# Kernel tuning notes

Measured on AMD Instinct MI355X. Metric: run time of the kernel, lower is better.

## Reference

```python
import jax, jax.numpy as jnp
import numpy as np

B, T, N, D = 8, 64, 128, 128  # batch, timesteps, num_nodes, hidden_dim
LN_EPS = 1e-5
L2_EPS = 1e-12


def setup_inputs() -> dict:
    key = jax.random.key(0)
    ks = jax.random.split(key, 8)
    feat = jax.random.normal(ks[0], (B, T, N, D), dtype=jnp.float32)
    w = jax.random.uniform(ks[1], (D,), dtype=jnp.float32)  # learned adj gate (torch.rand init)
    s = 1.0 / np.sqrt(D)
    W1 = jax.random.uniform(ks[2], (D, D), dtype=jnp.float32, minval=-s, maxval=s)
    b1 = jax.random.uniform(ks[3], (D,), dtype=jnp.float32, minval=-s, maxval=s)
    W2 = jax.random.uniform(ks[4], (D, D), dtype=jnp.float32, minval=-s, maxval=s)
    b2 = jax.random.uniform(ks[5], (D,), dtype=jnp.float32, minval=-s, maxval=s)
    gamma = jnp.ones((D,), dtype=jnp.float32)
    beta = jnp.zeros((D,), dtype=jnp.float32)
    return {"feat": feat, "w": w, "W1": W1, "b1": b1, "W2": W2, "b2": b2,
            "gamma": gamma, "beta": beta}


def _windows(x):
    # x: (B, T, N, D) -> (B, T-2, 3*N, D): 3 consecutive timesteps flattened over nodes
    b, t, n, d = x.shape
    return jnp.stack([x[:, i:i + t - 2] for i in range(3)], axis=2).reshape(b, t - 2, 3 * n, d)


def reference(feat, w, W1, b1, W2, b2, gamma, beta):
    # gated + L2-normalized features for learned adjacency
    wf = feat * jax.nn.sigmoid(w)
    wf = wf / jnp.maximum(jnp.linalg.norm(wf, axis=-1, keepdims=True), L2_EPS)

    win = _windows(feat)   # (B, T-2, 3N, D)
    wwin = _windows(wf)    # (B, T-2, 3N, D)

    # learned adjacency: gram matrix per window, (B, T-2, 3N, 3N)
    adj = jnp.einsum('btmd,btnd->btmn', wwin, wwin)

    # symmetric normalization D^{-1/2} A D^{-1/2}; inf/nan (deg<=0) -> 0 as in torch
    deg = adj.sum(axis=-1, keepdims=True)
    dis = jnp.where(deg > 0, jax.lax.rsqrt(jnp.maximum(deg, 1e-38)), 0.0)
    nadj = dis * adj * jnp.swapaxes(dis, -1, -2)

    # message passing, keep last N rows (current timestep)
    agg = jnp.einsum('btmn,btnd->btmd', nadj, win)[:, :, -N:, :]

    # FFN (dropout is identity in eval): Linear -> ReLU -> Linear
    h = jax.nn.relu(agg @ W1 + b1) @ W2 + b2

    # residual with current-timestep features + LayerNorm
    s = feat[:, 2:] + h
    mu = s.mean(axis=-1, keepdims=True)
    var = ((s - mu) ** 2).mean(axis=-1, keepdims=True)
    return (s - mu) * jax.lax.rsqrt(var + LN_EPS) * gamma + beta
```

## Files before the change

### kernel.cpp

```cpp
#include <hip/hip_runtime.h>
#include <math.h>

#define BB    8
#define TDIM  64
#define NN    128
#define DD    128
#define TTOUT 62
#define W3    384
#define LG    136
#define LP    40
#define LW    72

typedef __attribute__((ext_vector_type(8))) short bf16x8;
typedef __attribute__((ext_vector_type(4))) float f32x4;

__device__ __forceinline__ float sigf(float x){ return 1.0f/(1.0f+__expf(-x)); }
__device__ __forceinline__ unsigned short f2bf(float x){
  union{float f; unsigned u;} v; v.f=x;
  unsigned r = v.u + 0x7FFFu + ((v.u>>16)&1u);
  return (unsigned short)(r>>16);
}

__global__ __launch_bounds__(512) void k_pre(const float* __restrict__ feat,
    const float* __restrict__ w, const float* __restrict__ W1, const float* __restrict__ W2,
    float* __restrict__ rscale, float* __restrict__ ssum,
    unsigned short* __restrict__ W1T, unsigned short* __restrict__ W2T){
  __shared__ float sSig[DD];
  __shared__ float sRs[NN];
  __shared__ float sPart[4*DD];
  const int bid = blockIdx.x, tid = threadIdx.x;
  if(bid >= BB*TDIM){
    const float* W = (bid == BB*TDIM) ? W1 : W2;
    unsigned short* WT = (bid == BB*TDIM) ? W1T : W2T;
    for(int e=tid; e<DD*DD; e+=512){
      int k = e>>7, n = e&127;
      WT[n*DD + k] = f2bf(W[(size_t)k*DD + n]);
    }
    return;
  }
  const int bt = bid;
  if(tid < DD) sSig[tid] = sigf(w[tid]);
  __syncthreads();
  const int row = tid >> 2, q = tid & 3;
  const float* fp = feat + ((size_t)bt*NN + row)*DD + q*32;
  float ss = 0.f;
  #pragma unroll
  for(int i=0;i<8;i++){
    float4 v = *(const float4*)(fp + i*4);
    float g0 = v.x*sSig[q*32+i*4+0], g1 = v.y*sSig[q*32+i*4+1];
    float g2 = v.z*sSig[q*32+i*4+2], g3 = v.w*sSig[q*32+i*4+3];
    ss += g0*g0 + g1*g1 + g2*g2 + g3*g3;
  }
  ss += __shfl_xor(ss,1); ss += __shfl_xor(ss,2);
  float rs = 1.0f / fmaxf(sqrtf(ss), 1e-12f);
  if(q==0){ rscale[(size_t)bt*NN + row] = rs; sRs[row] = rs; }
  __syncthreads();
  const int d = tid & 127, rg = tid >> 7;
  const float* fc = feat + ((size_t)bt*NN + rg*32)*DD + d;
  float acc = 0.f;
  #pragma unroll 8
  for(int i=0;i<32;i++) acc += fc[(size_t)i*DD] * sRs[rg*32+i];
  sPart[rg*DD + d] = acc;
  __syncthreads();
  if(tid < DD)
    ssum[(size_t)bt*DD + tid] =
      (sPart[tid] + sPart[DD+tid] + sPart[2*DD+tid] + sPart[3*DD+tid]) * sSig[tid];
}

__global__ __launch_bounds__(512,4) void k_main(
    const float* __restrict__ feat,
    const float* __restrict__ w,
    const float* __restrict__ rscale, const float* __restrict__ ssum,
    const unsigned short* __restrict__ W1T, const float* __restrict__ b1,
    const unsigned short* __restrict__ W2T, const float* __restrict__ b2,
    const float* __restrict__ gamma, const float* __restrict__ beta,
    float* __restrict__ out)
{
  __shared__ __align__(16) unsigned short sm[32000];
  __shared__ float sSig[DD];
  __shared__ float s3c[DD];
  __shared__ float sFac[W3];
  unsigned short* sA  = sm;
  unsigned short* sG  = sm + 17408;
  unsigned short* sFt = sm + 21760;
  unsigned short* sP  = sm + 26880;
  unsigned short* sWt = sm + 17408;

  const int tid = threadIdx.x;
  const int bid = blockIdx.x;
  const int bt2 = (bid & 7)*62 + (bid >> 3);
  const int btIdx = (bt2/TTOUT)*TDIM + (bt2%TTOUT);
  const int rowBase = btIdx * NN;

  const int lane = tid & 63, wid = tid >> 6;
  const int l15 = lane & 15, l4 = lane >> 4;
  const int m0 = wid * 16;

  if(tid < DD){
    float sg = sigf(w[tid]);
    sSig[tid] = sg;
    float s3 = ssum[(size_t)btIdx*DD + tid] + ssum[(size_t)(btIdx+1)*DD + tid]
             + ssum[(size_t)(btIdx+2)*DD + tid];
    s3c[tid] = s3 * sg;
  }
  __syncthreads();

  #pragma unroll
  for(int rg=0; rg<3; ++rg){
    int row = rg*128 + (tid>>2), q = tid&3;
    const float* fpr = feat + (size_t)(rowBase+row)*DD + q*32;
    float a = 0.f;
    #pragma unroll
    for(int i=0;i<8;i++){
      float4 v = *(const float4*)(fpr + i*4);
      const float* sc = s3c + q*32 + i*4;
      a += v.x*sc[0] + v.y*sc[1] + v.z*sc[2] + v.w*sc[3];
    }
    a += __shfl_xor(a,1); a += __shfl_xor(a,2);
    if(q==0){
      float rs = rscale[rowBase+row];
      float deg = a * rs;
      float dis = (deg > 0.f) ? rsqrtf(fmaxf(deg, 1e-38f)) : 0.f;
      sFac[row] = dis * rs;
    }
  }
  __syncthreads();

  #pragma unroll
  for(int e0=0; e0<8; ++e0){
    int e = e0*512 + tid;
    int d = e & 127, r0 = (e>>7)*4;
    float sg = sSig[d];
    #pragma unroll
    for(int i=0;i<4;i++){
      int j = 256 + r0 + i;
      float f = feat[(size_t)(rowBase+j)*DD + d];
      sA[(r0+i)*LG + d] = f2bf(f*sg*sFac[j]);
    }
  }

  f32x4 acc2[8];
  #pragma unroll
  for(int i=0;i<8;i++) acc2[i] = (f32x4){0.f,0.f,0.f,0.f};

  for(int c=0; c<12; ++c){
    const int n0 = c*32;
    __syncthreads();
    #pragma unroll
    for(int e0=0; e0<2; ++e0){
      int e = e0*512 + tid;
      int d = e & 127, r0 = (e>>7)*4;
      float sg = sSig[d];
      unsigned short fb[4];
      #pragma unroll
      for(int i=0;i<4;i++){
        int j = n0 + r0 + i;
        float f = feat[(size_t)(rowBase+j)*DD + d];
        fb[i] = f2bf(f);
        sG[(r0+i)*LG + d] = f2bf(f*sg*sFac[j]);
      }
      unsigned int* fp = (unsigned int*)&sFt[d*LP + r0];
      fp[0] = (unsigned)fb[0] | ((unsigned)fb[1]<<16);
      fp[1] = (unsigned)fb[2] | ((unsigned)fb[3]<<16);
    }
    __syncthreads();

    f32x4 p0 = {0.f,0.f,0.f,0.f}, p1 = {0.f,0.f,0.f,0.f};
    #pragma unroll
    for(int ks=0; ks<4; ++ks){
      bf16x8 aA  = *(const bf16x8*)&sA[(m0+l15)*LG + ks*32 + l4*8];
      bf16x8 bg0 = *(const bf16x8*)&sG[( 0+l15)*LG + ks*32 + l4*8];
      bf16x8 bg1 = *(const bf16x8*)&sG[(16+l15)*LG + ks*32 + l4*8];
      p0 = __builtin_amdgcn_mfma_f32_16x16x32_bf16(aA, bg0, p0, 0,0,0);
      p1 = __builtin_amdgcn_mfma_f32_16x16x32_bf16(aA, bg1, p1, 0,0,0);
    }
    #pragma unroll
    for(int r=0;r<4;r++){
      sP[(m0 + l4*4 + r)*LP +  0 + l15] = f2bf(p0[r]);
      sP[(m0 + l4*4 + r)*LP + 16 + l15] = f2bf(p1[r]);
    }

    bf16x8 aP = *(const bf16x8*)&sP[(m0+l15)*LP + l4*8];
    #pragma unroll
    for(int dt=0; dt<8; ++dt){
      bf16x8 bF = *(const bf16x8*)&sFt[(dt*16+l15)*LP + l4*8];
      acc2[dt] = __builtin_amdgcn_mfma_f32_16x16x32_bf16(aP, bF, acc2[dt], 0,0,0);
    }
  }

  #pragma unroll
  for(int dt=0; dt<8; ++dt)
    #pragma unroll
    for(int r=0;r<4;r++)
      sA[(m0+l4*4+r)*LG + dt*16+l15] = f2bf(acc2[dt][r]);

  f32x4 acch[8];
  #pragma unroll
  for(int dt=0; dt<8; ++dt){
    float bv = b1[dt*16+l15];
    acch[dt] = (f32x4){bv,bv,bv,bv};
  }
  for(int kh=0; kh<2; ++kh){
    __syncthreads();
    #pragma unroll
    for(int it=0; it<2; ++it){
      int e = it*512 + tid, n = e>>3, sg2 = e&7;
      uint4 v = *(const uint4*)(W1T + (size_t)n*DD + kh*64 + sg2*8);
      *(uint4*)&sWt[n*LW + sg2*8] = v;
    }
    __syncthreads();
    #pragma unroll
    for(int ks=0; ks<2; ++ks){
      bf16x8 aA = *(const bf16x8*)&sA[(m0+l15)*LG + kh*64 + ks*32 + l4*8];
      #pragma unroll
      for(int dt=0; dt<8; ++dt){
        bf16x8 bW = *(const bf16x8*)&sWt[(dt*16+l15)*LW + ks*32 + l4*8];
        acch[dt] = __builtin_amdgcn_mfma_f32_16x16x32_bf16(aA, bW, acch[dt], 0,0,0);
      }
    }
  }
  __syncthreads();
  #pragma unroll
  for(int dt=0; dt<8; ++dt)
    #pragma unroll
    for(int r=0;r<4;r++)
      sA[(m0+l4*4+r)*LG + dt*16+l15] = f2bf(fmaxf(acch[dt][r], 0.f));

  f32x4 acco[8];
  #pragma unroll
  for(int dt=0; dt<8; ++dt){
    float bv = b2[dt*16+l15];
    acco[dt] = (f32x4){bv,bv,bv,bv};
  }
  for(int kh=0; kh<2; ++kh){
    __syncthreads();
    #pragma unroll
    for(int it=0; it<2; ++it){
      int e = it*512 + tid, n = e>>3, sg2 = e&7;
      uint4 v = *(const uint4*)(W2T + (size_t)n*DD + kh*64 + sg2*8);
      *(uint4*)&sWt[n*LW + sg2*8] = v;
    }
    __syncthreads();
    #pragma unroll
    for(int ks=0; ks<2; ++ks){
      bf16x8 aA = *(const bf16x8*)&sA[(m0+l15)*LG + kh*64 + ks*32 + l4*8];
      #pragma unroll
      for(int dt=0; dt<8; ++dt){
        bf16x8 bW = *(const bf16x8*)&sWt[(dt*16+l15)*LW + ks*32 + l4*8];
        acco[dt] = __builtin_amdgcn_mfma_f32_16x16x32_bf16(aA, bW, acco[dt], 0,0,0);
      }
    }
  }

  const float* fres = feat + (size_t)(rowBase + 256)*DD;
  #pragma unroll
  for(int r=0;r<4;r++){
    int m = m0 + l4*4 + r;
    float vals[8]; float s1 = 0.f, s2 = 0.f;
    #pragma unroll
    for(int dt=0; dt<8; ++dt){
      int d = dt*16 + l15;
      float v = acco[dt][r] + fres[(size_t)m*DD + d];
      vals[dt] = v; s1 += v; s2 += v*v;
    }
    #pragma unroll
    for(int k=1;k<16;k<<=1){ s1 += __shfl_xor(s1,k); s2 += __shfl_xor(s2,k); }
    float mu   = s1*(1.0f/DD);
    float rstd = rsqrtf(s2*(1.0f/DD) - mu*mu + 1e-5f);
    #pragma unroll
    for(int dt=0; dt<8; ++dt){
      int d = dt*16 + l15;
      out[((size_t)bt2*NN + m)*DD + d] = (vals[dt]-mu)*rstd*gamma[d] + beta[d];
    }
  }
}

extern "C" void kernel_launch(void* const* d_in, const int* in_sizes, int n_in,
                              void* d_out, int out_size, void* d_ws, size_t ws_size,
                              hipStream_t stream){
  const float* feat  = (const float*)d_in[0];
  const float* w     = (const float*)d_in[1];
  const float* W1    = (const float*)d_in[2];
  const float* b1    = (const float*)d_in[3];
  const float* W2    = (const float*)d_in[4];
  const float* b2    = (const float*)d_in[5];
  const float* gamma = (const float*)d_in[6];
  const float* beta  = (const float*)d_in[7];
  float* out = (float*)d_out;

  char* ws = (char*)d_ws;
  float* rscale = (float*)(ws + 0);
  float* ssum   = (float*)(ws + 262144);
  unsigned short* W1T = (unsigned short*)(ws + 524288);
  unsigned short* W2T = (unsigned short*)(ws + 557056);

  k_pre<<<BB*TDIM + 2, 512, 0, stream>>>(feat, w, W1, W2, rscale, ssum, W1T, W2T);
  k_main<<<BB*TTOUT, 512, 0, stream>>>(feat, w, rscale, ssum, W1T, b1, W2T, b2,
                                       gamma, beta, out);
}
```

Measured before the change: 81.36 us.

## Double k_main block to 1024 threads, splitting output columns across wave halves

Each block now runs 16 waves instead of 8. Each pair of waves shares a 16-row strip and splits the output columns (D tiles and the 32-wide P chunk) in half, which halves per-wave accumulator registers and the MFMA work per wave. This aims to raise in-CU parallelism and latency hiding. In exchange it adds one more block-wide barrier per chunk iteration and an LDS round-trip to combine the LayerNorm partial sums across the two halves.

Result: slower. 94.31 us (+15.9%).

```diff
diff --git a/kernel.cpp b/kernel.cpp
--- a/kernel.cpp
+++ b/kernel.cpp
@@ -67,7 +67,7 @@
       (sPart[tid] + sPart[DD+tid] + sPart[2*DD+tid] + sPart[3*DD+tid]) * sSig[tid];
 }
 
-__global__ __launch_bounds__(512,4) void k_main(
+__global__ __launch_bounds__(1024,2) void k_main(
     const float* __restrict__ feat,
     const float* __restrict__ w,
     const float* __restrict__ rscale, const float* __restrict__ ssum,
@@ -80,6 +80,7 @@
   __shared__ float sSig[DD];
   __shared__ float s3c[DD];
   __shared__ float sFac[W3];
+  __shared__ float sLN[NN*4];
   unsigned short* sA  = sm;
   unsigned short* sG  = sm + 17408;
   unsigned short* sFt = sm + 21760;
@@ -94,7 +95,9 @@
 
   const int lane = tid & 63, wid = tid >> 6;
   const int l15 = lane & 15, l4 = lane >> 4;
-  const int m0 = wid * 16;
+  const int s  = wid & 7,  h = wid >> 3;
+  const int m0 = s * 16;
+  const int dt0 = h * 4;
 
   if(tid < DD){
     float sg = sigf(w[tid]);
@@ -106,29 +109,32 @@
   __syncthreads();
 
   #pragma unroll
-  for(int rg=0; rg<3; ++rg){
-    int row = rg*128 + (tid>>2), q = tid&3;
-    const float* fpr = feat + (size_t)(rowBase+row)*DD + q*32;
-    float a = 0.f;
-    #pragma unroll
-    for(int i=0;i<8;i++){
-      float4 v = *(const float4*)(fpr + i*4);
-      const float* sc = s3c + q*32 + i*4;
-      a += v.x*sc[0] + v.y*sc[1] + v.z*sc[2] + v.w*sc[3];
-    }
-    a += __shfl_xor(a,1); a += __shfl_xor(a,2);
-    if(q==0){
-      float rs = rscale[rowBase+row];
-      float deg = a * rs;
-      float dis = (deg > 0.f) ? rsqrtf(fmaxf(deg, 1e-38f)) : 0.f;
-      sFac[row] = dis * rs;
-    }
-  }
-  __syncthreads();
-
-  #pragma unroll
-  for(int e0=0; e0<8; ++e0){
-    int e = e0*512 + tid;
+  for(int rg=0; rg<2; ++rg){
+    int row = rg*256 + (tid>>2);
+    if(row < W3){
+      int q = tid & 3;
+      const float* fpr = feat + (size_t)(rowBase+row)*DD + q*32;
+      float a = 0.f;
+      #pragma unroll
+      for(int i=0;i<8;i++){
+        float4 v = *(const float4*)(fpr + i*4);
+        const float* sc = s3c + q*32 + i*4;
+        a += v.x*sc[0] + v.y*sc[1] + v.z*sc[2] + v.w*sc[3];
+      }
+      a += __shfl_xor(a,1); a += __shfl_xor(a,2);
+      if(q==0){
+        float rs = rscale[rowBase+row];
+        float deg = a * rs;
+        float dis = (deg > 0.f) ? rsqrtf(fmaxf(deg, 1e-38f)) : 0.f;
+        sFac[row] = dis * rs;
+      }
+    }
+  }
+  __syncthreads();
+
+  #pragma unroll
+  for(int e0=0; e0<4; ++e0){
+    int e = e0*1024 + tid;
     int d = e & 127, r0 = (e>>7)*4;
     float sg = sSig[d];
     #pragma unroll
@@ -139,17 +145,15 @@
     }
   }
 
-  f32x4 acc2[8];
-  #pragma unroll
-  for(int i=0;i<8;i++) acc2[i] = (f32x4){0.f,0.f,0.f,0.f};
+  f32x4 acc2[4];
+  #pragma unroll
+  for(int i=0;i<4;i++) acc2[i] = (f32x4){0.f,0.f,0.f,0.f};
 
   for(int c=0; c<12; ++c){
     const int n0 = c*32;
     __syncthreads();
-    #pragma unroll
-    for(int e0=0; e0<2; ++e0){
-      int e = e0*512 + tid;
-      int d = e & 127, r0 = (e>>7)*4;
+    {
+      int d = tid & 127, r0 = (tid>>7)*4;
       float sg = sSig[d];
       unsigned short fb[4];
       #pragma unroll
@@ -165,46 +169,42 @@
     }
     __syncthreads();
 
-    f32x4 p0 = {0.f,0.f,0.f,0.f}, p1 = {0.f,0.f,0.f,0.f};
+    f32x4 p = {0.f,0.f,0.f,0.f};
     #pragma unroll
     for(int ks=0; ks<4; ++ks){
-      bf16x8 aA  = *(const bf16x8*)&sA[(m0+l15)*LG + ks*32 + l4*8];
-      bf16x8 bg0 = *(const bf16x8*)&sG[( 0+l15)*LG + ks*32 + l4*8];
-      bf16x8 bg1 = *(const bf16x8*)&sG[(16+l15)*LG + ks*32 + l4*8];
-      p0 = __builtin_amdgcn_mfma_f32_16x16x32_bf16(aA, bg0, p0, 0,0,0);
-      p1 = __builtin_amdgcn_mfma_f32_16x16x32_bf16(aA, bg1, p1, 0,0,0);
-    }
-    #pragma unroll
-    for(int r=0;r<4;r++){
-      sP[(m0 + l4*4 + r)*LP +  0 + l15] = f2bf(p0[r]);
-      sP[(m0 + l4*4 + r)*LP + 16 + l15] = f2bf(p1[r]);
-    }
+      bf16x8 aA = *(const bf16x8*)&sA[(m0+l15)*LG + ks*32 + l4*8];
+      bf16x8 bg = *(const bf16x8*)&sG[(h*16+l15)*LG + ks*32 + l4*8];
+      p = __builtin_amdgcn_mfma_f32_16x16x32_bf16(aA, bg, p, 0,0,0);
+    }
+    #pragma unroll
+    for(int r=0;r<4;r++)
+      sP[(m0 + l4*4 + r)*LP + h*16 + l15] = f2bf(p[r]);
+    __syncthreads();
 
     bf16x8 aP = *(const bf16x8*)&sP[(m0+l15)*LP + l4*8];
     #pragma unroll
-    for(int dt=0; dt<8; ++dt){
-      bf16x8 bF = *(const bf16x8*)&sFt[(dt*16+l15)*LP + l4*8];
-      acc2[dt] = __builtin_amdgcn_mfma_f32_16x16x32_bf16(aP, bF, acc2[dt], 0,0,0);
-    }
-  }
-
-  #pragma unroll
-  for(int dt=0; dt<8; ++dt)
+    for(int dtl=0; dtl<4; ++dtl){
+      bf16x8 bF = *(const bf16x8*)&sFt[((dt0+dtl)*16+l15)*LP + l4*8];
+      acc2[dtl] = __builtin_amdgcn_mfma_f32_16x16x32_bf16(aP, bF, acc2[dtl], 0,0,0);
+    }
+  }
+
+  #pragma unroll
+  for(int dtl=0; dtl<4; ++dtl)
     #pragma unroll
     for(int r=0;r<4;r++)
-      sA[(m0+l4*4+r)*LG + dt*16+l15] = f2bf(acc2[dt][r]);
-
-  f32x4 acch[8];
-  #pragma unroll
-  for(int dt=0; dt<8; ++dt){
-    float bv = b1[dt*16+l15];
-    acch[dt] = (f32x4){bv,bv,bv,bv};
+      sA[(m0+l4*4+r)*LG + (dt0+dtl)*16+l15] = f2bf(acc2[dtl][r]);
+
+  f32x4 acch[4];
+  #pragma unroll
+  for(int dtl=0; dtl<4; ++dtl){
+    float bv = b1[(dt0+dtl)*16+l15];
+    acch[dtl] = (f32x4){bv,bv,bv,bv};
   }
   for(int kh=0; kh<2; ++kh){
     __syncthreads();
-    #pragma unroll
-    for(int it=0; it<2; ++it){
-      int e = it*512 + tid, n = e>>3, sg2 = e&7;
+    {
+      int n = tid>>3, sg2 = tid&7;
       uint4 v = *(const uint4*)(W1T + (size_t)n*DD + kh*64 + sg2*8);
       *(uint4*)&sWt[n*LW + sg2*8] = v;
     }
@@ -213,30 +213,29 @@
     for(int ks=0; ks<2; ++ks){
       bf16x8 aA = *(const bf16x8*)&sA[(m0+l15)*LG + kh*64 + ks*32 + l4*8];
       #pragma unroll
-      for(int dt=0; dt<8; ++dt){
-        bf16x8 bW = *(const bf16x8*)&sWt[(dt*16+l15)*LW + ks*32 + l4*8];
-        acch[dt] = __builtin_amdgcn_mfma_f32_16x16x32_bf16(aA, bW, acch[dt], 0,0,0);
-      }
-    }
-  }
-  __syncthreads();
-  #pragma unroll
-  for(int dt=0; dt<8; ++dt)
+      for(int dtl=0; dtl<4; ++dtl){
+        bf16x8 bW = *(const bf16x8*)&sWt[((dt0+dtl)*16+l15)*LW + ks*32 + l4*8];
+        acch[dtl] = __builtin_amdgcn_mfma_f32_16x16x32_bf16(aA, bW, acch[dtl], 0,0,0);
+      }
+    }
+  }
+  __syncthreads();
+  #pragma unroll
+  for(int dtl=0; dtl<4; ++dtl)
     #pragma unroll
     for(int r=0;r<4;r++)
-      sA[(m0+l4*4+r)*LG + dt*16+l15] = f2bf(fmaxf(acch[dt][r], 0.f));
-
-  f32x4 acco[8];
-  #pragma unroll
-  for(int dt=0; dt<8; ++dt){
-    float bv = b2[dt*16+l15];
-    acco[dt] = (f32x4){bv,bv,bv,bv};
+      sA[(m0+l4*4+r)*LG + (dt0+dtl)*16+l15] = f2bf(fmaxf(acch[dtl][r], 0.f));
+
+  f32x4 acco[4];
+  #pragma unroll
+  for(int dtl=0; dtl<4; ++dtl){
+    float bv = b2[(dt0+dtl)*16+l15];
+    acco[dtl] = (f32x4){bv,bv,bv,bv};
   }
   for(int kh=0; kh<2; ++kh){
     __syncthreads();
-    #pragma unroll
-    for(int it=0; it<2; ++it){
-      int e = it*512 + tid, n = e>>3, sg2 = e&7;
+    {
+      int n = tid>>3, sg2 = tid&7;
       uint4 v = *(const uint4*)(W2T + (size_t)n*DD + kh*64 + sg2*8);
       *(uint4*)&sWt[n*LW + sg2*8] = v;
     }
@@ -245,9 +244,9 @@
     for(int ks=0; ks<2; ++ks){
       bf16x8 aA = *(const bf16x8*)&sA[(m0+l15)*LG + kh*64 + ks*32 + l4*8];
       #pragma unroll
-      for(int dt=0; dt<8; ++dt){
-        bf16x8 bW = *(const bf16x8*)&sWt[(dt*16+l15)*LW + ks*32 + l4*8];
-        acco[dt] = __builtin_amdgcn_mfma_f32_16x16x32_bf16(aA, bW, acco[dt], 0,0,0);
+      for(int dtl=0; dtl<4; ++dtl){
+        bf16x8 bW = *(const bf16x8*)&sWt[((dt0+dtl)*16+l15)*LW + ks*32 + l4*8];
+        acco[dtl] = __builtin_amdgcn_mfma_f32_16x16x32_bf16(aA, bW, acco[dtl], 0,0,0);
       }
     }
   }
@@ -256,21 +255,30 @@
   #pragma unroll
   for(int r=0;r<4;r++){
     int m = m0 + l4*4 + r;
-    float vals[8]; float s1 = 0.f, s2 = 0.f;
-    #pragma unroll
-    for(int dt=0; dt<8; ++dt){
-      int d = dt*16 + l15;
-      float v = acco[dt][r] + fres[(size_t)m*DD + d];
-      vals[dt] = v; s1 += v; s2 += v*v;
+    float s1 = 0.f, s2 = 0.f;
+    #pragma unroll
+    for(int dtl=0; dtl<4; ++dtl){
+      int d = (dt0+dtl)*16 + l15;
+      float v = acco[dtl][r] + fres[(size_t)m*DD + d];
+      acco[dtl][r] = v;
+      s1 += v; s2 += v*v;
     }
     #pragma unroll
     for(int k=1;k<16;k<<=1){ s1 += __shfl_xor(s1,k); s2 += __shfl_xor(s2,k); }
+    if(l15==0){ sLN[m*4 + h*2] = s1; sLN[m*4 + h*2 + 1] = s2; }
+  }
+  __syncthreads();
+  #pragma unroll
+  for(int r=0;r<4;r++){
+    int m = m0 + l4*4 + r;
+    float s1 = sLN[m*4] + sLN[m*4+2];
+    float s2 = sLN[m*4+1] + sLN[m*4+3];
     float mu   = s1*(1.0f/DD);
     float rstd = rsqrtf(s2*(1.0f/DD) - mu*mu + 1e-5f);
     #pragma unroll
-    for(int dt=0; dt<8; ++dt){
-      int d = dt*16 + l15;
-      out[((size_t)bt2*NN + m)*DD + d] = (vals[dt]-mu)*rstd*gamma[d] + beta[d];
+    for(int dtl=0; dtl<4; ++dtl){
+      int d = (dt0+dtl)*16 + l15;
+      out[((size_t)bt2*NN + m)*DD + d] = (acco[dtl][r]-mu)*rstd*gamma[d] + beta[d];
     }
   }
 }
@@ -295,6 +303,6 @@
   unsigned short* W2T = (unsigned short*)(ws + 557056);
 
   k_pre<<<BB*TDIM + 2, 512, 0, stream>>>(feat, w, W1, W2, rscale, ssum, W1T, W2T);
-  k_main<<<BB*TTOUT, 512, 0, stream>>>(feat, w, rscale, ssum, W1T, b1, W2T, b2,
-                                       gamma, beta, out);
+  k_main<<<BB*TTOUT, 1024, 0, stream>>>(feat, w, rscale, ssum, W1T, b1, W2T, b2,
+                                        gamma, beta, out);
 }
```
